# Kernel tuning notes

Hardware: AMD Instinct MI355X
Metric: run time of the kernel (lower is better)

## Reference

```python
import jax, jax.numpy as jnp
import numpy as np

N = 20000; DX = 512; DW = 64; DY = 256; M = 320000
DS = DX // 2; DD = DX // 4; DP = DS + DD  # 256, 128, 384
EPS = 1e-9; LN_EPS = 1e-5; SLOPE = 0.05
PNAMES = ['rW1','rb1','rg1','rbt1','rW2','rb2','yW1','yb1','yg1','ybt1','yW2','yb2',
          'iaW1','iab1','iag1','iabt1','iaW2','iab2','cW1','cb1','cg1','cbt1','cW2','cb2']

def _mlp2(h, W1, b1, g, be, W2, b2):
    # Linear -> LayerNorm -> LeakyReLU(0.05) -> Linear  (matches mlp(..., norm='layer'))
    h = h @ W1 + b1
    mu = jnp.mean(h, axis=-1, keepdims=True)
    var = jnp.mean((h - mu) ** 2, axis=-1, keepdims=True)
    h = (h - mu) * jax.lax.rsqrt(var + LN_EPS) * g + be
    h = jnp.where(h >= 0, h, SLOPE * h)
    return h @ W2 + b2

def _m(Pp, n, h):
    return _mlp2(h, Pp[n+'W1'], Pp[n+'b1'], Pp[n+'g1'], Pp[n+'bt1'], Pp[n+'W2'], Pp[n+'b2'])

def _agg(a, b):
    s = a + b
    return jnp.where(s >= 0, s, SLOPE * s)

def _run(x, ei, edge_attr, u_r, u_ia, u_pick, Pp, dec=None):
    """GuoUnpool forward (steps 1a, 2a, 2b). ei: concrete numpy [2,M] int64.
    dec holds concrete sampled decisions; built from the uniforms when None."""
    build = dec is None
    if build:
        dec = {}
    # coalesce (edges are duplicate-free) + lexsort by (src, dst)
    perm = np.argsort(ei[0].astype(np.int64) * N + ei[1].astype(np.int64), kind='stable')
    src, dst = ei[0][perm], ei[1][perm]
    ea = edge_attr[perm]
    # --- step 1a: bernoulli unpool decision per node (I_s = I_u = empty, I_r = all nodes)
    pr = jax.nn.sigmoid(_m(Pp, 'r', x)[:, 0])
    if build:
        dec['choose'] = np.asarray(u_r) < np.asarray(pr)
    choose = dec['choose']
    Iu = np.flatnonzero(choose); Is = np.flatnonzero(~choose)
    logP = jnp.sum(jnp.where(jnp.asarray(choose), jnp.log(pr + EPS), jnp.log(1.0 - pr + EPS)))
    prs = jnp.clip(pr, EPS, 1.0 - EPS)
    ent = -jnp.sum(prs * jnp.log(prs) + (1.0 - prs) * jnp.log(1.0 - prs))
    # --- projections (_ps1_idx = [0:ds+D], _ps2_idx = [0:ds] + [ds+D:ds+2D]) and child embeddings
    ps1 = x[:, :DP]
    ps2 = jnp.concatenate([x[:, :DS], x[:, DS + DD:DS + 2 * DD]], axis=-1)
    y1 = _m(Pp, 'y', ps1)   # [N, dy]; rows at Is give x_static, rows at Iu give x_c1
    y2 = _m(Pp, 'y', ps2)   # rows at Iu give x_c2
    x_out = jnp.concatenate([y1[Is], y1[Iu], y2[Iu]], axis=0)
    # --- step 2a: intra-edge decision for unpooled nodes
    p_ia = jax.nn.sigmoid(_m(Pp, 'ia', _agg(y1[Iu], y2[Iu]))[:, 0])
    if build:
        dec['vc'] = np.asarray(u_ia)[Iu] < np.asarray(p_ia)
    vc = dec['vc']
    logP = logP + jnp.sum(jnp.where(jnp.asarray(vc), jnp.log(p_ia + EPS), jnp.log(1.0 - p_ia + EPS)))
    ps = jnp.clip(p_ia, EPS, 1.0 - EPS)
    ent = ent - jnp.sum(ps * jnp.log(ps) + (1.0 - ps) * jnp.log(1.0 - ps))
    # --- step 2b: categorical neighbor pick for unpooled nodes without intra edge
    if build:
        iun = Iu[~vc]
        par = np.concatenate([src, dst]); nb = np.concatenate([dst, src])
        ek = np.concatenate([np.arange(len(src)), np.arange(len(src))])
        keep = np.zeros(N, dtype=bool); keep[iun] = True
        msk = keep[par]
        par, nb, ek = par[msk], nb[msk], ek[msk]
        o = np.lexsort((nb, par))  # adj lists sorted by neighbor id, grouped by parent
        par, nb, ek = par[o], nb[o], ek[o]
        new = np.r_[True, par[1:] != par[:-1]]
        dec['par'], dec['nb'], dec['ek'] = par, nb, ek
        dec['seg'] = np.cumsum(new) - 1
        dec['starts'] = np.flatnonzero(new)
    par, nb, ek = dec['par'], dec['nb'], dec['ek']
    segn, starts = dec['seg'], dec['starts']
    Pn = len(par); nseg = int(segn[-1]) + 1
    seg = jnp.asarray(segn)
    yagg = _agg(y1, y2)
    feats = jnp.concatenate([yagg[par], ea[ek], x[nb]], axis=-1)  # [Pn, dy+dw+dx]
    scores = _m(Pp, 'c', feats)[:, 0]
    mx = jax.ops.segment_max(scores, seg, num_segments=nseg)
    e = jnp.exp(scores - mx[segn])
    den = jax.ops.segment_sum(e, seg, num_segments=nseg)
    probs = e / den[segn]                      # per-parent softmax over neighbors
    if build:
        # multinomial pick via inverse CDF on the provided per-parent uniform
        p_np = np.asarray(probs).astype(np.float64)
        cum = np.cumsum(p_np)
        base = np.concatenate([[0.0], cum])[starts]
        cumw = cum - base[segn]
        useg = np.asarray(u_pick)[par[starts]][segn]
        cand = np.where(cumw > useg, np.arange(Pn), Pn)
        pick = np.minimum.reduceat(cand, starts)
        last = np.r_[starts[1:] - 1, Pn - 1]
        dec['pick'] = np.minimum(pick, last)
    pick = dec['pick']
    logP = logP + jnp.sum(jnp.log(jnp.clip(probs[pick], EPS, None)))
    pc = jnp.clip(probs, EPS, None)
    ent = ent - jnp.sum(pc * jnp.log(pc))
    return (x_out, logP, ent), dec

def _init_params(key):
    Pp = {}
    specs = [('r', DX, max(1, DX // 2), 1), ('y', DP, 128, DY), ('ia', DY, 128, 1), ('c', DY + DW + DX, 128, 1)]
    ks = jax.random.split(key, len(specs))
    for (n, a, h, o), k in zip(specs, ks):
        k1, k2 = jax.random.split(k)
        Pp[n+'W1'] = jax.random.normal(k1, (a, h), jnp.float32) / np.sqrt(a)
        Pp[n+'b1'] = jnp.zeros((h,), jnp.float32)
        Pp[n+'g1'] = jnp.ones((h,), jnp.float32)
        Pp[n+'bt1'] = jnp.zeros((h,), jnp.float32)
        Pp[n+'W2'] = jax.random.normal(k2, (h, o), jnp.float32) / np.sqrt(h)
        Pp[n+'b2'] = jnp.zeros((o,), jnp.float32)
    return Pp

def setup_inputs() -> dict:
    key = jax.random.key(0)
    k = jax.random.split(key, 6)
    x = jax.random.normal(k[0], (N, DX), jnp.float32)
    rng = np.random.default_rng(0)
    ns = int(M * 1.5)
    s = rng.integers(0, N, ns); d = rng.integers(0, N, ns)
    ok = s != d; s, d = s[ok], d[ok]
    _, ui = np.unique(s.astype(np.int64) * N + d, return_index=True)  # duplicate-free (coalesced)
    sel = rng.permutation(ui)[:M]
    edge_index = jnp.asarray(np.stack([s[sel], d[sel]]).astype(np.int64))
    inp = {
        'x': x,
        'edge_index': edge_index,
        'edge_attr': 0.5 * jax.random.normal(k[1], (M, DW), jnp.float32),
        'u_r': jax.random.uniform(k[2], (N,), jnp.float32),
        'u_ia': jax.random.uniform(k[3], (N,), jnp.float32),
        'u_pick': jax.random.uniform(k[4], (N,), jnp.float32),
    }
    inp.update(_init_params(k[5]))
    return inp

def reference(x, edge_index, edge_attr, u_r, u_ia, u_pick,
              rW1, rb1, rg1, rbt1, rW2, rb2,
              yW1, yb1, yg1, ybt1, yW2, yb2,
              iaW1, iab1, iag1, iabt1, iaW2, iab2,
              cW1, cb1, cg1, cbt1, cW2, cb2):
    Pp = dict(zip(PNAMES, (rW1, rb1, rg1, rbt1, rW2, rb2, yW1, yb1, yg1, ybt1, yW2, yb2,
                           iaW1, iab1, iag1, iabt1, iaW2, iab2, cW1, cb1, cg1, cbt1, cW2, cb2)))
    out, _ = _run(x, np.asarray(edge_index), edge_attr, u_r, u_ia, u_pick, Pp)
    return out
```

## Files before the change

kernel.cpp:

```cpp
#include <hip/hip_runtime.h>
#include <math.h>

#define KN 20000
#define KM 320000

typedef __attribute__((ext_vector_type(8))) short bf16x8;
typedef __attribute__((ext_vector_type(4))) float f32x4;

__device__ __forceinline__ ushort f2bf(float f){
  union{float f; unsigned u;} a; a.f=f;
  unsigned r = a.u + 0x7FFFu + ((a.u>>16)&1u);
  return (ushort)(r>>16);
}
__device__ __forceinline__ float bf2f(ushort u){
  union{unsigned u; float f;} a; a.u=((unsigned)u)<<16; return a.f;
}

__device__ __forceinline__ void blk_add2(double lp, double en, double* acc, double* sh){
#pragma unroll
  for (int o=32;o;o>>=1){ lp+=__shfl_xor(lp,o,64); en+=__shfl_xor(en,o,64); }
  int w=threadIdx.x>>6;
  if ((threadIdx.x&63)==0){ sh[2*w]=lp; sh[2*w+1]=en; }
  __syncthreads();
  if (threadIdx.x==0){
    double L=0,E=0; int nw=(blockDim.x+63)>>6;
    for (int i=0;i<nw;i++){L+=sh[2*i];E+=sh[2*i+1];}
    atomicAdd(&acc[0],L); atomicAdd(&acc[1],E);
  }
  __syncthreads();
}

__global__ __launch_bounds__(256) void k_prep_all(
    const float* __restrict__ x, ushort* __restrict__ x_hi, ushort* __restrict__ x_lo,
    const float* __restrict__ Wr1, ushort* __restrict__ Wrt_hi, ushort* __restrict__ Wrt_lo,
    double* __restrict__ w1d,
    const float* __restrict__ Wc1, ushort* __restrict__ W1t,
    const float* __restrict__ Wy1, ushort* __restrict__ W1yt,
    const float* __restrict__ Wy2, ushort* __restrict__ W2yt,
    int* __restrict__ deg,int* __restrict__ fill,int* __restrict__ keep,
    int* __restrict__ counters,double* __restrict__ acc){
  int i=blockIdx.x*256+threadIdx.x;
  if (i<KN*512/8){
    const float* s=x+(size_t)i*8;
    union{ushort u[8]; uint4 v;} oh, ol;
#pragma unroll
    for (int j=0;j<8;j++){
      float v=s[j];
      ushort h=f2bf(v);
      oh.u[j]=h;
      ol.u[j]=f2bf(v-bf2f(h));
    }
    *(uint4*)(x_hi+(size_t)i*8)=oh.v;
    *(uint4*)(x_lo+(size_t)i*8)=ol.v;
  }
  if (i<512*256){
    w1d[i]=(double)Wr1[i];
    int n=i&255, k=i>>8;
    float wv=Wr1[(size_t)k*256+n];
    ushort h=f2bf(wv);
    int kt=k>>5, kc=(k>>3)&3, j=k&7;
    size_t dst=(((size_t)kt*1024)+(size_t)kc*256+(size_t)n)*8+j;
    Wrt_hi[dst]=h;
    Wrt_lo[dst]=f2bf(wv-bf2f(h));
  }
  if (i<832*128){
    int n=i&127, k=i>>7;
    W1t[(size_t)n*832+k]=f2bf(Wc1[(size_t)k*128+n]);
  }
  if (i<384*128){
    int n=i&127, k=i>>7;
    W1yt[(size_t)n*384+k]=f2bf(Wy1[(size_t)k*128+n]);
  }
  if (i<128*256){
    int n=i&255, k=i>>8;
    W2yt[(size_t)n*128+k]=f2bf(Wy2[(size_t)k*256+n]);
  }
  if (i<KN){ deg[i]=0; fill[i]=0; keep[i]=0; }
  if (i<8) counters[i]=0;
  if (i<2) acc[i]=0.0;
}

#define RFLAG_TAU 3e-4f
#define YEXTP 261
__global__ __launch_bounds__(512) void k_mega1(const float* __restrict__ x,
    const ushort* __restrict__ x_hi,const ushort* __restrict__ x_lo,
    const ushort* __restrict__ Wrt_hi,const ushort* __restrict__ Wrt_lo,
    const double* __restrict__ w1d,
    const float* __restrict__ b1,const float* __restrict__ g1,
    const float* __restrict__ bt1,const float* __restrict__ W2,const float* __restrict__ b2,
    const float* __restrict__ u_r, float* __restrict__ pr, int* __restrict__ choose,
    const ushort* __restrict__ W1t, float* __restrict__ hxP,
    const ushort* __restrict__ W1yt,const float* __restrict__ b1y,const float* __restrict__ g1y,
    const float* __restrict__ bt1y,const ushort* __restrict__ W2yt,const float* __restrict__ b2y,
    float* __restrict__ y1_f,float* __restrict__ y2_f,
    float* __restrict__ yagg_f,ushort* __restrict__ yagg_bf,
    int RB,int HXB){
  __shared__ __align__(16) ushort Bl[2][2][8192];
  __shared__ float psum[64][2], pvar[64][2], pdot[64][2];
  __shared__ int flagsh[64];
  __shared__ double dsh[256];
  int t=threadIdx.x;
  int w=t>>6, l=t&63;
  int lr=l&15, lk=l>>4;
  if ((int)blockIdx.x>=RB+HXB){
    int b=blockIdx.x-RB-HXB;
    int sub=t>>8, tt=t&255;
    char* gbase=(char*)Bl + sub*25600;
    float*  hf  =(float*)gbase;
    float*  yext=(float*)gbase;
    ushort* hb  =(ushort*)(gbase+16896);
    int wy=tt>>6, ly=tt&63;
    int lry=ly&15, lky=ly>>4;
    int md=wy&1, kh=wy>>1;
    int row0=(b*2+sub)*16;
    const ushort* xr=x_hi+(size_t)(row0+lry)*512;
    f32x4 acc1[8];
#pragma unroll
    for (int c=0;c<8;c++) acc1[c]=(f32x4){0,0,0,0};
#pragma unroll
    for (int kt=0;kt<6;kt++){
      int k0=kh*192+kt*32+lky*8;
      int ks=(md && k0>=256)? k0+128 : k0;
      bf16x8 a=*(const bf16x8*)(xr+ks);
#pragma unroll
      for (int c=0;c<8;c++){
        bf16x8 b_=*(const bf16x8*)(W1yt+(size_t)(c*16+lry)*384+k0);
        acc1[c]=__builtin_amdgcn_mfma_f32_16x16x32_bf16(a,b_,acc1[c],0,0,0);
      }
    }
    if (kh==0){
#pragma unroll
      for (int i=0;i<4;i++){
        int row=lky*4+i;
#pragma unroll
        for (int c=0;c<8;c++) hf[((size_t)md*16+row)*132+c*16+lry]=acc1[c][i];
      }
    }
    __syncthreads();
    if (kh==1){
      float b1v[8],g1v[8],btv[8];
#pragma unroll
      for (int c=0;c<8;c++){ int col=c*16+lry; b1v[c]=b1y[col]; g1v[c]=g1y[col]; btv[c]=bt1y[col]; }
#pragma unroll
      for (int i=0;i<4;i++){
        int row=lky*4+i;
        float hv[8]; float s=0.f;
#pragma unroll
        for (int c=0;c<8;c++){ hv[c]=acc1[c][i]+hf[((size_t)md*16+row)*132+c*16+lry]+b1v[c]; s+=hv[c]; }
#pragma unroll
        for (int o=8;o;o>>=1) s+=__shfl_xor(s,o,64);
        float mu=s*(1.0f/128.0f);
        float v=0.f;
#pragma unroll
        for (int c=0;c<8;c++){ float d=hv[c]-mu; v+=d*d; }
#pragma unroll
        for (int o=8;o;o>>=1) v+=__shfl_xor(v,o,64);
        float rs=1.0f/sqrtf(v*(1.0f/128.0f)+1e-5f);
        ushort* hrow=hb+((size_t)md*16+row)*136;
#pragma unroll
        for (int c=0;c<8;c++){
          float hn=(hv[c]-mu)*rs*g1v[c]+btv[c];
          hn=hn>=0.f?hn:0.05f*hn;
          hrow[c*16+lry]=f2bf(hn);
        }
      }
    }
    __syncthreads();
    f32x4 acc2[8];
#pragma unroll
    for (int c=0;c<8;c++) acc2[c]=(f32x4){0,0,0,0};
    const ushort* ha=hb+((size_t)md*16+lry)*136;
#pragma unroll
    for (int kt=0;kt<4;kt++){
      bf16x8 a=*(const bf16x8*)(ha+kt*32+lky*8);
#pragma unroll
      for (int c=0;c<8;c++){
        bf16x8 b_=*(const bf16x8*)(W2yt+(size_t)(kh*128+c*16+lry)*128+kt*32+lky*8);
        acc2[c]=__builtin_amdgcn_mfma_f32_16x16x32_bf16(a,b_,acc2[c],0,0,0);
      }
    }
    float b2v[8];
#pragma unroll
    for (int c=0;c<8;c++) b2v[c]=b2y[kh*128+c*16+lry];
    if (md==0){
#pragma unroll
      for (int i=0;i<4;i++){
        int row=lky*4+i;
#pragma unroll
        for (int c=0;c<8;c++) yext[(size_t)row*YEXTP+kh*128+c*16+lry]=acc2[c][i]+b2v[c];
      }
    }
    __syncthreads();
    if (md==0){
#pragma unroll
      for (int i=0;i<4;i++){
        int row=lky*4+i, n=row0+row;
        float* orow=y1_f+(size_t)n*256+kh*128;
#pragma unroll
        for (int c=0;c<8;c++) orow[c*16+lry]=acc2[c][i]+b2v[c];
      }
    } else {
#pragma unroll
      for (int i=0;i<4;i++){
        int row=lky*4+i, n=row0+row;
        size_t base=(size_t)n*256+kh*128;
#pragma unroll
        for (int c=0;c<8;c++){
          int colk=c*16+lry;
          float v2=acc2[c][i]+b2v[c];
          float v1=yext[(size_t)row*YEXTP+kh*128+colk];
          float ga=v1+v2; ga=ga>=0.f?ga:0.05f*ga;
          yagg_f[base+colk]=ga;
          yagg_bf[base+colk]=f2bf(ga);
          y2_f[base+colk]=v2;
        }
      }
    }
    return;
  }
  if ((int)blockIdx.x>=RB){
    int b2=blockIdx.x-RB;
    int rh=w>>2, cw=w&3;
    int row0=b2*32+rh*16;
    const ushort* ar=x_hi+(size_t)(row0+lr)*512;
    f32x4 acc3[2];
#pragma unroll
    for (int c=0;c<2;c++) acc3[c]=(f32x4){0,0,0,0};
#pragma unroll
    for (int kt=0;kt<16;kt++){
      bf16x8 a=*(const bf16x8*)(ar+320+kt*32+lk*8);
#pragma unroll
      for (int c=0;c<2;c++){
        bf16x8 b=*(const bf16x8*)(W1t+(size_t)(cw*32+c*16+lr)*832+320+kt*32+lk*8);
        acc3[c]=__builtin_amdgcn_mfma_f32_16x16x32_bf16(a,b,acc3[c],0,0,0);
      }
    }
#pragma unroll
    for (int i=0;i<4;i++){
      int n=row0+lk*4+i;
      float2 v; v.x=acc3[0][i]; v.y=acc3[1][i];
      *(float2*)(hxP+(size_t)n*128+lr*8+cw*2)=v;
    }
    return;
  }
  int rg=w>>1, ch=w&1;
  int row0=blockIdx.x*64;
  if (t<64) flagsh[t]=0;
  int q0=t*2, q1=t*2+1;
  f32x4 acc[8];
#pragma unroll
  for (int c=0;c<8;c++) acc[c]=(f32x4){0,0,0,0};
  int rowA=row0+rg*16+lr; if (rowA>=KN) rowA=KN-1;
  const ushort* ah=x_hi+(size_t)rowA*512;
  const ushort* al=x_lo+(size_t)rowA*512;
  bf16x8 nh0=*(const bf16x8*)(Wrt_hi+q0*8);
  bf16x8 nh1=*(const bf16x8*)(Wrt_hi+q1*8);
  bf16x8 nl0=*(const bf16x8*)(Wrt_lo+q0*8);
  bf16x8 nl1=*(const bf16x8*)(Wrt_lo+q1*8);
  *(bf16x8*)&Bl[0][0][q0*8]=nh0; *(bf16x8*)&Bl[0][0][q1*8]=nh1;
  *(bf16x8*)&Bl[0][1][q0*8]=nl0; *(bf16x8*)&Bl[0][1][q1*8]=nl1;
  nh0=*(const bf16x8*)(Wrt_hi+8192+q0*8);
  nh1=*(const bf16x8*)(Wrt_hi+8192+q1*8);
  nl0=*(const bf16x8*)(Wrt_lo+8192+q0*8);
  nl1=*(const bf16x8*)(Wrt_lo+8192+q1*8);
  bf16x8 a_h0=*(const bf16x8*)(ah+0*32+lk*8), a_l0=*(const bf16x8*)(al+0*32+lk*8);
  bf16x8 a_h1=*(const bf16x8*)(ah+1*32+lk*8), a_l1=*(const bf16x8*)(al+1*32+lk*8);
  bf16x8 a_h2=*(const bf16x8*)(ah+2*32+lk*8), a_l2=*(const bf16x8*)(al+2*32+lk*8);
  bf16x8 a_h3=*(const bf16x8*)(ah+3*32+lk*8), a_l3=*(const bf16x8*)(al+3*32+lk*8);
  __syncthreads();
#define RBODY(KT,AH,AL) { \
    const int cur_=(KT)&1, nxt_=cur_^1; \
    if ((KT)<15){ \
      *(bf16x8*)&Bl[nxt_][0][q0*8]=nh0; *(bf16x8*)&Bl[nxt_][0][q1*8]=nh1; \
      *(bf16x8*)&Bl[nxt_][1][q0*8]=nl0; *(bf16x8*)&Bl[nxt_][1][q1*8]=nl1; \
      if ((KT)<14){ \
        size_t so_=(size_t)((KT)+2)*8192; \
        nh0=*(const bf16x8*)(Wrt_hi+so_+q0*8); nh1=*(const bf16x8*)(Wrt_hi+so_+q1*8); \
        nl0=*(const bf16x8*)(Wrt_lo+so_+q0*8); nl1=*(const bf16x8*)(Wrt_lo+so_+q1*8); \
      } \
    } \
    bf16x8 uh_=AH, ul_=AL; \
    if ((KT)<12){ \
      int ko_=((KT)+4)*32+lk*8; \
      AH=*(const bf16x8*)(ah+ko_); \
      AL=*(const bf16x8*)(al+ko_); \
    } \
    _Pragma("unroll") \
    for (int c=0;c<8;c++){ \
      int col_=ch*128+c*16+lr; \
      bf16x8 vh_=*(const bf16x8*)&Bl[cur_][0][((lk<<8)+col_)*8]; \
      bf16x8 vl_=*(const bf16x8*)&Bl[cur_][1][((lk<<8)+col_)*8]; \
      acc[c]=__builtin_amdgcn_mfma_f32_16x16x32_bf16(uh_,vh_,acc[c],0,0,0); \
      acc[c]=__builtin_amdgcn_mfma_f32_16x16x32_bf16(uh_,vl_,acc[c],0,0,0); \
      acc[c]=__builtin_amdgcn_mfma_f32_16x16x32_bf16(ul_,vh_,acc[c],0,0,0); \
    } \
    __syncthreads(); \
  }
  RBODY(0,a_h0,a_l0)  RBODY(1,a_h1,a_l1)  RBODY(2,a_h2,a_l2)  RBODY(3,a_h3,a_l3)
  RBODY(4,a_h0,a_l0)  RBODY(5,a_h1,a_l1)  RBODY(6,a_h2,a_l2)  RBODY(7,a_h3,a_l3)
  RBODY(8,a_h0,a_l0)  RBODY(9,a_h1,a_l1)  RBODY(10,a_h2,a_l2) RBODY(11,a_h3,a_l3)
  RBODY(12,a_h0,a_l0) RBODY(13,a_h1,a_l1) RBODY(14,a_h2,a_l2) RBODY(15,a_h3,a_l3)
#undef RBODY
  float b1v[8],g1v[8],btv[8],w2v[8];
#pragma unroll
  for (int c=0;c<8;c++){
    int col=ch*128+c*16+lr;
    b1v[c]=b1[col]; g1v[c]=g1[col]; btv[c]=bt1[col]; w2v[c]=W2[col];
  }
  float hv[4][8];
#pragma unroll
  for (int i=0;i<4;i++){
    float s=0.f;
#pragma unroll
    for (int c=0;c<8;c++){ hv[i][c]=acc[c][i]+b1v[c]; s+=hv[i][c]; }
#pragma unroll
    for (int o=8;o;o>>=1) s+=__shfl_xor(s,o,64);
    if (lr==0) psum[rg*16+lk*4+i][ch]=s;
  }
  __syncthreads();
  float mu_[4];
#pragma unroll
  for (int i=0;i<4;i++){
    int r=rg*16+lk*4+i;
    mu_[i]=(psum[r][0]+psum[r][1])*(1.0f/256.0f);
    float v=0.f;
#pragma unroll
    for (int c=0;c<8;c++){ float d=hv[i][c]-mu_[i]; v+=d*d; }
#pragma unroll
    for (int o=8;o;o>>=1) v+=__shfl_xor(v,o,64);
    if (lr==0) pvar[r][ch]=v;
  }
  __syncthreads();
#pragma unroll
  for (int i=0;i<4;i++){
    int r=rg*16+lk*4+i;
    float rs=1.0f/sqrtf((pvar[r][0]+pvar[r][1])*(1.0f/256.0f)+1e-5f);
    float dot=0.f;
#pragma unroll
    for (int c=0;c<8;c++){
      float hn=(hv[i][c]-mu_[i])*rs*g1v[c]+btv[c];
      hn=hn>=0.f?hn:0.05f*hn;
      dot=fmaf(hn,w2v[c],dot);
    }
#pragma unroll
    for (int o=8;o;o>>=1) dot+=__shfl_xor(dot,o,64);
    if (lr==0) pdot[r][ch]=dot;
  }
  __syncthreads();
  if (t<64){
    int n=row0+t;
    if (n<KN){
      float o2=pdot[t][0]+pdot[t][1]+b2[0];
      float pf=1.0f/(1.0f+expf(-o2));
      float u=u_r[n];
      pr[n]=pf;
      choose[n]=(u<pf)?1:0;
      if (fabsf(pf-u)<RFLAG_TAU) flagsh[t]=1;
    }
  }
  __syncthreads();
  for (int r=0;r<64;r++){
    if (!flagsh[r]) continue;
    int n=row0+r;
    if (t<256){
      double ha=(double)b1[t];
      const float* xr=x+(size_t)n*512;
      for (int k=0;k<512;k++) ha=fma((double)xr[k],w1d[(size_t)k*256+t],ha);
      dsh[t]=ha;
    }
    __syncthreads();
    if (t<64){
      double s=0;
      for (int j=t;j<256;j+=64) s+=dsh[j];
#pragma unroll
      for (int o=32;o;o>>=1) s+=__shfl_xor(s,o,64);
      double mu=s*(1.0/256.0);
      double v=0;
      for (int j=t;j<256;j+=64){ double d=dsh[j]-mu; v+=d*d; }
#pragma unroll
      for (int o=32;o;o>>=1) v+=__shfl_xor(v,o,64);
      double rs=1.0/sqrt(v*(1.0/256.0)+1e-5);
      double dot=0;
      for (int j=t;j<256;j+=64){
        double hn=(dsh[j]-mu)*rs*(double)g1[j]+(double)bt1[j];
        hn = hn>=0.0? hn : 0.05*hn;
        dot=fma(hn,(double)W2[j],dot);
      }
#pragma unroll
      for (int o=32;o;o>>=1) dot+=__shfl_xor(dot,o,64);
      if (t==0){
        double p=1.0/(1.0+exp(-(dot+(double)b2[0])));
        float pf=(float)p;
        pr[n]=pf;
        choose[n]=(u_r[n]<pf)?1:0;
      }
    }
    __syncthreads();
  }
}

__global__ __launch_bounds__(1024) void k_scan_choose(const int* __restrict__ choose,int* __restrict__ excl,
                                                      int* __restrict__ iu,int* __restrict__ counters){
  __shared__ int wsum[16], woff[16];
  const int CH=(KN+1023)/1024;
  int t=threadIdx.x, lane=t&63, wid=t>>6;
  int base=t*CH;
  int s=0;
  for (int i=0;i<CH;i++){int idx=base+i; if (idx<KN) s+=choose[idx];}
  int inc=s;
  for (int o=1;o<64;o<<=1){ int v=__shfl_up(inc,o,64); if (lane>=o) inc+=v; }
  if (lane==63) wsum[wid]=inc;
  __syncthreads();
  if (t==0){ int r=0; for (int i=0;i<16;i++){ woff[i]=r; r+=wsum[i]; } counters[2]=r; }
  __syncthreads();
  int ex=woff[wid]+inc-s;
  for (int i=0;i<CH;i++){
    int idx=base+i;
    if (idx<KN){ int c=choose[idx]; excl[idx]=ex; if (c) iu[ex]=idx; ex+=c; }
  }
}

__global__ __launch_bounds__(256) void k_mega2(const float* __restrict__ yagg_f,
    const ushort* __restrict__ yagg_bf,const ushort* __restrict__ W1t,float* __restrict__ hyP,
    const int* __restrict__ iu,const float* __restrict__ u_ia,
    const float* __restrict__ W1,const float* __restrict__ b1,const float* __restrict__ g1,
    const float* __restrict__ bt1,const float* __restrict__ W2,const float* __restrict__ b2,
    float* __restrict__ p_ia,int* __restrict__ vc,int* __restrict__ keep,double* __restrict__ acc,
    const float* __restrict__ y1_f,const float* __restrict__ y2_f,
    const int* __restrict__ choose,const int* __restrict__ excl,
    float* __restrict__ out,const float* __restrict__ pr,
    int cnt,int HB,int IAB,int SCB){
  __shared__ float insh[16][256];
  __shared__ float hsh[16][128];
  __shared__ double sh[8];
  int t=threadIdx.x;
  int w=t>>6, l=t&63;
  int lr=l&15, lk=l>>4;
  if ((int)blockIdx.x<HB){
    int rh=w>>1, cq=w&1;
    int row0=blockIdx.x*32+rh*16;
    const ushort* ar=yagg_bf+(size_t)(row0+lr)*256+lk*8;
    f32x4 acc4[4];
#pragma unroll
    for (int c=0;c<4;c++) acc4[c]=(f32x4){0,0,0,0};
#pragma unroll
    for (int kt=0;kt<8;kt++){
      bf16x8 a=*(const bf16x8*)(ar+kt*32);
#pragma unroll
      for (int c=0;c<4;c++){
        bf16x8 b=*(const bf16x8*)(W1t+(size_t)(cq*64+c*16+lr)*832+kt*32+lk*8);
        acc4[c]=__builtin_amdgcn_mfma_f32_16x16x32_bf16(a,b,acc4[c],0,0,0);
      }
    }
#pragma unroll
    for (int i=0;i<4;i++){
      int n=row0+lk*4+i;
      float4 v; v.x=acc4[0][i]; v.y=acc4[1][i]; v.z=acc4[2][i]; v.w=acc4[3][i];
      *(float4*)(hyP+(size_t)n*128+lr*8+cq*4)=v;
    }
    return;
  }
  if ((int)blockIdx.x<HB+IAB){
    int row0=(blockIdx.x-HB)*16;
    for (int i=t;i<16*256;i+=256){
      int r=i>>8,k=i&255;
      int row=row0+r;
      if (row<cnt){
        unsigned n=(unsigned)iu[row];
        if (n<KN) insh[r][k]=yagg_f[(size_t)n*256+k];
        else insh[r][k]=0.f;
      }
    }
    __syncthreads();
    int h=t>>7, tt=t&127;
    float accv[8]; float bb=b1[tt];
#pragma unroll
    for (int r=0;r<8;r++) accv[r]=bb;
    for (int k=0;k<256;k+=4){
      float w0=W1[(k+0)*128+tt],w1=W1[(k+1)*128+tt],w2=W1[(k+2)*128+tt],w3=W1[(k+3)*128+tt];
#pragma unroll
      for (int r=0;r<8;r++){
        float4 f=*(const float4*)&insh[h*8+r][k];
        accv[r]=fmaf(f.x,w0,accv[r]); accv[r]=fmaf(f.y,w1,accv[r]); accv[r]=fmaf(f.z,w2,accv[r]); accv[r]=fmaf(f.w,w3,accv[r]);
      }
    }
#pragma unroll
    for (int r=0;r<8;r++) hsh[h*8+r][tt]=accv[r];
    __syncthreads();
    int g=t>>4, tl=t&15;
    float hv[8];
#pragma unroll
    for (int j=0;j<8;j++) hv[j]=hsh[g][tl+16*j];
    float s=0;
#pragma unroll
    for (int j=0;j<8;j++) s+=hv[j];
#pragma unroll
    for (int o=8;o;o>>=1) s+=__shfl_xor(s,o,64);
    float mu=s*(1.0f/128.0f);
    float v=0;
#pragma unroll
    for (int j=0;j<8;j++){float d=hv[j]-mu; v+=d*d;}
#pragma unroll
    for (int o=8;o;o>>=1) v+=__shfl_xor(v,o,64);
    float rs=1.0f/sqrtf(v*(1.0f/128.0f)+1e-5f);
    float dot=0;
#pragma unroll
    for (int j=0;j<8;j++){
      int idx=tl+16*j;
      float hn=(hv[j]-mu)*rs*g1[idx]+bt1[idx];
      hn=hn>=0.f?hn:0.05f*hn;
      dot=fmaf(hn,W2[idx],dot);
    }
#pragma unroll
    for (int o=8;o;o>>=1) dot+=__shfl_xor(dot,o,64);
    double lp=0,en=0;
    if (tl==0){
      int row=row0+g;
      if (row<cnt){
        unsigned n=(unsigned)iu[row];
        if (n<KN){
          float o=dot+b2[0];
          double p=1.0/(1.0+exp(-(double)o));
          float pf=(float)p;
          p_ia[row]=pf;
          int vv=(u_ia[n]<pf)?1:0;
          vc[row]=vv;
          if(!vv) keep[n]=1;
          lp = vv? log((double)pf+1e-9) : log(1.0-(double)pf+1e-9);
          double ps=fmin(fmax((double)pf,1e-9),1.0-1e-9);
          en = -(ps*log(ps)+(1.0-ps)*log(1.0-ps));
        }
      }
    }
    blk_add2(lp,en,acc,sh);
    return;
  }
  if ((int)blockIdx.x<HB+IAB+SCB){
    int b=blockIdx.x-HB-IAB;
    int r0=b*32;
    for (int r=0;r<32;r++){
      int n=r0+r;
      if (n>=KN) break;
      int cch=choose[n], ex=excl[n];
      int r1 = cch? (KN-cnt)+ex : n-ex;
      if (r1>=0 && r1<KN+cnt) out[(size_t)r1*256+t]=y1_f[(size_t)n*256+t];
      if (cch){ int r2=KN+ex; if (r2<KN+cnt) out[(size_t)r2*256+t]=y2_f[(size_t)n*256+t]; }
    }
    return;
  }
  {
    int i=(blockIdx.x-HB-IAB-SCB)*256+t;
    double lp=0,en=0;
    if (i<KN){
      double p=(double)pr[i];
      lp = choose[i]? log(p+1e-9) : log(1.0-p+1e-9);
      double ps=fmin(fmax(p,1e-9),1.0-1e-9);
      en = -(ps*log(ps)+(1.0-ps)*log(1.0-ps));
    }
    blk_add2(lp,en,acc,(double*)insh);
  }
}

__global__ void k_count(const int* __restrict__ ei,const int* __restrict__ keep,int* __restrict__ deg){
  int e=blockIdx.x*256+threadIdx.x;
  if (e<KM){
    int s=ei[e], d=ei[KM+e];
    if (keep[s]) atomicAdd(&deg[s],1);
    if (keep[d]) atomicAdd(&deg[d],1);
  }
}

__global__ __launch_bounds__(1024) void k_scan_deg(const int* __restrict__ deg,int* __restrict__ boff,
                                                   int* __restrict__ nodeseg,int* __restrict__ counters){
  __shared__ int wsum[16], woff[16];
  const int CH=(KN+1023)/1024;
  int t=threadIdx.x, lane=t&63, wid=t>>6;
  int base=t*CH;
  int s=0, sc=0;
  for (int i=0;i<CH;i++){int idx=base+i; if(idx<KN){ int d=deg[idx]; s+=d; sc+=(d>0)?1:0; }}
  int inc=s;
  for (int o=1;o<64;o<<=1){ int v=__shfl_up(inc,o,64); if (lane>=o) inc+=v; }
  if (lane==63) wsum[wid]=inc;
  __syncthreads();
  if (t==0){ int r=0; for (int i=0;i<16;i++){ woff[i]=r; r+=wsum[i]; } boff[KN]=r; counters[0]=r; }
  __syncthreads();
  int ex=woff[wid]+inc-s;
  for (int i=0;i<CH;i++){int idx=base+i; if(idx<KN){ boff[idx]=ex; ex+=deg[idx]; }}
  __syncthreads();
  int inc2=sc;
  for (int o=1;o<64;o<<=1){ int v=__shfl_up(inc2,o,64); if (lane>=o) inc2+=v; }
  if (lane==63) wsum[wid]=inc2;
  __syncthreads();
  if (t==0){ int r=0; for (int i=0;i<16;i++){ woff[i]=r; r+=wsum[i]; } counters[1]=r; }
  __syncthreads();
  int ex2=woff[wid]+inc2-sc;
  for (int i=0;i<CH;i++){int idx=base+i; if(idx<KN && deg[idx]>0){ nodeseg[ex2]=idx; ex2++; }}
}

__global__ void k_fill(const int* __restrict__ ei,const int* __restrict__ keep,const int* __restrict__ boff,
                       int* __restrict__ fill,int* __restrict__ parA,int* __restrict__ keyA,int* __restrict__ ekA){
  int e=blockIdx.x*256+threadIdx.x;
  if (e<KM){
    int s=ei[e], d=ei[KM+e];
    if (keep[s]){ int pos=boff[s]+atomicAdd(&fill[s],1); parA[pos]=s; keyA[pos]=d*2;   ekA[pos]=e; }
    if (keep[d]){ int pos=boff[d]+atomicAdd(&fill[d],1); parA[pos]=d; keyA[pos]=s*2+1; ekA[pos]=e; }
  }
}

__global__ void k_rank(const int* __restrict__ parA,const int* __restrict__ keyA,const int* __restrict__ ekA,
                       const int* __restrict__ boff,const int* __restrict__ counters,
                       int* __restrict__ parS,int* __restrict__ nbS,int* __restrict__ ekS){
  int i=blockIdx.x*256+threadIdx.x;
  int Pn=counters[0];
  if (i<Pn){
    int par=parA[i], key=keyA[i];
    int lo=boff[par], hi=boff[par+1];
    int rank=0;
    for (int j=lo;j<hi;j++) rank += (keyA[j]<key)?1:0;
    int pos=lo+rank;
    parS[pos]=par; nbS[pos]=key>>1; ekS[pos]=ekA[i];
  }
}

__global__ __launch_bounds__(256) void k_cscore_v6(
    const float* __restrict__ ea,const float* __restrict__ hyP,const float* __restrict__ hxP,
    const int* __restrict__ parS,const int* __restrict__ nbS,const int* __restrict__ ekS,
    const int* __restrict__ counters,
    const ushort* __restrict__ W1t,const float* __restrict__ b1,const float* __restrict__ g1,
    const float* __restrict__ bt1,const float* __restrict__ W2,const float* __restrict__ b2,
    float* __restrict__ scores){
  int Pn=counters[0];
  if (Pn<=0) return;
  int t=threadIdx.x;
  int w=t>>6, l=t&63;
  int lr=l&15, lk=l>>4;
  float b2s=b2[0];
  float b1v[8],g1v[8],btv[8],w2v[8];
#pragma unroll
  for (int c=0;c<8;c++){
    int col=c*16+lr;
    b1v[c]=b1[col]; g1v[c]=g1[col]; btv[c]=bt1[col]; w2v[c]=W2[col];
  }
  int ngrp=(Pn+63)>>6;
  for (int g=blockIdx.x; g<ngrp; g+=gridDim.x){
    int p0=g*64+w*16;
    float hs[4][8];
#pragma unroll
    for (int i=0;i<4;i++){
      int p=p0+lk*4+i; int pc=p<Pn?p:Pn-1;
      const float* hyp=hyP+(size_t)parS[pc]*128+lr*8;
      const float* hxp=hxP+(size_t)nbS[pc]*128+lr*8;
      float4 ya=*(const float4*)hyp, yb=*(const float4*)(hyp+4);
      float4 xa=*(const float4*)hxp, xb=*(const float4*)(hxp+4);
      hs[i][0]=ya.x+xa.x; hs[i][1]=ya.y+xa.y; hs[i][2]=ya.z+xa.z; hs[i][3]=ya.w+xa.w;
      hs[i][4]=yb.x+xb.x; hs[i][5]=yb.y+xb.y; hs[i][6]=yb.z+xb.z; hs[i][7]=yb.w+xb.w;
    }
    int pA=p0+lr; int ca=pA<Pn?pA:Pn-1;
    const float* eaA=ea+(size_t)ekS[ca]*64;
    f32x4 acc[8];
#pragma unroll
    for (int c=0;c<8;c++) acc[c]=(f32x4){0,0,0,0};
#pragma unroll
    for (int kt=0;kt<2;kt++){
      float4 fa=*(const float4*)(eaA+kt*32+lk*8);
      float4 fb=*(const float4*)(eaA+kt*32+lk*8+4);
      union{ushort u[8]; bf16x8 v;} A;
      A.u[0]=f2bf(fa.x); A.u[1]=f2bf(fa.y); A.u[2]=f2bf(fa.z); A.u[3]=f2bf(fa.w);
      A.u[4]=f2bf(fb.x); A.u[5]=f2bf(fb.y); A.u[6]=f2bf(fb.z); A.u[7]=f2bf(fb.w);
      bf16x8 a=A.v;
#pragma unroll
      for (int c=0;c<8;c++){
        bf16x8 b=*(const bf16x8*)(W1t+(size_t)(c*16+lr)*832+256+kt*32+lk*8);
        acc[c]=__builtin_amdgcn_mfma_f32_16x16x32_bf16(a,b,acc[c],0,0,0);
      }
    }
#pragma unroll
    for (int i=0;i<4;i++){
      float hv[8]; float s=0.f;
#pragma unroll
      for (int c=0;c<8;c++){ hv[c]=acc[c][i]+hs[i][c]+b1v[c]; s+=hv[c]; }
#pragma unroll
      for (int o=8;o;o>>=1) s+=__shfl_xor(s,o,64);
      float mu=s*(1.0f/128.0f);
      float v=0.f;
#pragma unroll
      for (int c=0;c<8;c++){ float d=hv[c]-mu; v+=d*d; }
#pragma unroll
      for (int o=8;o;o>>=1) v+=__shfl_xor(v,o,64);
      float rs=1.0f/sqrtf(v*(1.0f/128.0f)+1e-5f);
      float dot=0.f;
#pragma unroll
      for (int c=0;c<8;c++){
        float hn=(hv[c]-mu)*rs*g1v[c]+btv[c];
        hn=hn>=0.f?hn:0.05f*hn;
        dot=fmaf(hn,w2v[c],dot);
      }
#pragma unroll
      for (int o=8;o;o>>=1) dot+=__shfl_xor(dot,o,64);
      if (lr==0){
        int prow=p0+lk*4+i;
        if (prow<Pn) scores[prow]=dot+b2s;
      }
    }
  }
}

__global__ __launch_bounds__(256) void k_segment(const float* __restrict__ scores,const int* __restrict__ boff,
    const int* __restrict__ nodeseg,int* __restrict__ counters,const float* __restrict__ u_pick,
    double* __restrict__ acc,float* __restrict__ out,int cnt){
  __shared__ double sh[8];
  int nseg=counters[1];
  int s=blockIdx.x*256+threadIdx.x;
  double lp=0,en=0;
  if (s<nseg){
    int n=nodeseg[s];
    int lo=boff[n],hi=boff[n+1];
    float mx=-1e30f;
    for (int p=lo;p<hi;p++) mx=fmaxf(mx,scores[p]);
    float den=0;
    for (int p=lo;p<hi;p++) den+=expf(scores[p]-mx);
    double u=(double)u_pick[n];
    double cum=0; float ppick=-1.f; float plast=0.f;
    for (int p=lo;p<hi;p++){
      float e=expf(scores[p]-mx);
      float prob=e/den;
      double pc=fmax((double)prob,1e-9);
      en -= pc*log(pc);
      plast=prob;
      if (ppick<0.f){ cum+=(double)prob; if (cum>u) ppick=prob; }
    }
    if (ppick<0.f) ppick=plast;
    lp=log(fmax((double)ppick,1e-9));
  }
  blk_add2(lp,en,acc,sh);
  if (threadIdx.x==0){
    __threadfence();
    int done=atomicAdd(&counters[3],1);
    if (done==(int)gridDim.x-1){
      __threadfence();
      size_t base=(size_t)(KN+cnt)*256;
      out[base]=(float)acc[0];
      out[base+1]=(float)acc[1];
    }
  }
}

extern "C" void kernel_launch(void* const* d_in,const int* in_sizes,int n_in,
                              void* d_out,int out_size,void* d_ws,size_t ws_size,
                              hipStream_t stream){
  const float* x     =(const float*)d_in[0];
  const int*   ei    =(const int*)  d_in[1];
  const float* ea    =(const float*)d_in[2];
  const float* u_r   =(const float*)d_in[3];
  const float* u_ia  =(const float*)d_in[4];
  const float* u_pick=(const float*)d_in[5];
  const float* Pp[24];
  for (int i=0;i<24;i++) Pp[i]=(const float*)d_in[6+i];
  float* out=(float*)d_out;
  int cnt=(out_size-2)/256 - KN;
  if (cnt<0) cnt=0;

  char* w=(char*)d_ws;
  size_t off=0;
  auto carve=[&](size_t bytes)->char*{ off=(off+255)&~(size_t)255; char* p=w+off; off+=bytes; return p; };
  int*    counters=(int*)   carve(64);
  double* acc     =(double*)carve(64);
  float*  pr      =(float*) carve((size_t)KN*4);
  int*    choose  =(int*)   carve((size_t)KN*4);
  int*    excl    =(int*)   carve((size_t)KN*4);
  int*    iu      =(int*)   carve((size_t)KN*4);
  float*  p_ia    =(float*) carve((size_t)KN*4);
  int*    vc      =(int*)   carve((size_t)KN*4);
  int*    keep    =(int*)   carve((size_t)KN*4);
  int*    deg     =(int*)   carve((size_t)KN*4);
  int*    fill    =(int*)   carve((size_t)KN*4);
  int*    boff    =(int*)   carve((size_t)(KN+1)*4);
  int*    nodeseg =(int*)   carve((size_t)KN*4);
  int*    parA    =(int*)   carve((size_t)2*KM*4);
  int*    keyA    =(int*)   carve((size_t)2*KM*4);
  int*    ekA     =(int*)   carve((size_t)2*KM*4);
  int*    parS    =(int*)   carve((size_t)2*KM*4);
  int*    nbS     =(int*)   carve((size_t)2*KM*4);
  int*    ekS     =(int*)   carve((size_t)2*KM*4);
  float*  scores  =(float*) carve((size_t)2*KM*4);
  float*  yagg_f  =(float*) carve((size_t)KN*256*4);
  ushort* yagg_bf =(ushort*)carve((size_t)KN*256*2);
  float*  y1_f    =(float*) carve((size_t)KN*256*4);
  float*  y2_f    =(float*) carve((size_t)KN*256*4);
  ushort* x_bf    =(ushort*)carve((size_t)KN*512*2);
  ushort* x_lo    =(ushort*)carve((size_t)KN*512*2);
  ushort* W1t     =(ushort*)carve((size_t)832*128*2);
  double* w1d     =(double*)carve((size_t)512*256*8);
  ushort* W1yt    =(ushort*)carve((size_t)128*384*2);
  ushort* W2yt    =(ushort*)carve((size_t)256*128*2);
  ushort* Wrt_hi  =(ushort*)carve((size_t)256*512*2);
  ushort* Wrt_lo  =(ushort*)carve((size_t)256*512*2);
  float*  hy      =(float*) carve((size_t)KN*128*4);
  float*  hx      =(float*) carve((size_t)KN*128*4);
  (void)ws_size;(void)n_in;(void)in_sizes;

  const int RB=(KN+63)/64;
  const int HXB=KN/32;
  const int YB2=KN/32;
  const int HB=KN/32;
  const int IAB=(cnt+15)/16;
  const int SCB=(KN+31)/32;
  const int NTB=(KN+255)/256;

  k_prep_all<<<(KN*512/8+255)/256,256,0,stream>>>(x,x_bf,x_lo,
      Pp[0],Wrt_hi,Wrt_lo,w1d, Pp[18],W1t, Pp[6],W1yt, Pp[10],W2yt,
      deg,fill,keep,counters,acc);
  k_mega1<<<RB+HXB+YB2,512,0,stream>>>(x,x_bf,x_lo,Wrt_hi,Wrt_lo,w1d,
      Pp[1],Pp[2],Pp[3],Pp[4],Pp[5],u_r,pr,choose,W1t,hx,
      W1yt,Pp[7],Pp[8],Pp[9],W2yt,Pp[11],y1_f,y2_f,yagg_f,yagg_bf,RB,HXB);
  k_scan_choose<<<1,1024,0,stream>>>(choose,excl,iu,counters);
  k_mega2<<<HB+IAB+SCB+NTB,256,0,stream>>>(yagg_f,yagg_bf,W1t,hy,iu,u_ia,
      Pp[12],Pp[13],Pp[14],Pp[15],Pp[16],Pp[17],p_ia,vc,keep,acc,
      y1_f,y2_f,choose,excl,out,pr,cnt,HB,IAB,SCB);
  k_count<<<(KM+255)/256,256,0,stream>>>(ei,keep,deg);
  k_scan_deg<<<1,1024,0,stream>>>(deg,boff,nodeseg,counters);
  k_fill<<<(KM+255)/256,256,0,stream>>>(ei,keep,boff,fill,parA,keyA,ekA);
  k_rank<<<(2*KM+255)/256,256,0,stream>>>(parA,keyA,ekA,boff,counters,parS,nbS,ekS);
  k_cscore_v6<<<2560,256,0,stream>>>(ea,hy,hx,parS,nbS,ekS,counters,W1t,Pp[19],Pp[20],Pp[21],Pp[22],Pp[23],scores);
  k_segment<<<(KN+255)/256,256,0,stream>>>(scores,boff,nodeseg,counters,u_pick,acc,out,cnt);
}
```

Before: 407.8 us.

## Fuse edge-sort, scoring and segment-softmax tail into one cooperative kernel

Replaces the six tail kernels (degree count, degree scan, fill, rank, edge scoring and segment softmax) with a single cooperative kernel. The stages are separated by grid-wide syncs and use grid-stride loops, with the grid sized from occupancy and cached in a static. This removes several launch gaps and kernel-boundary drains. In exchange it adds grid.sync costs, moves the degree scan onto one 256-thread block instead of 1024 threads, and may give the scoring stage fewer resident blocks than before.

```diff
diff --git a/kernel.cpp b/kernel.cpp
--- a/kernel.cpp
+++ b/kernel.cpp
@@ -1,8 +1,11 @@
 #include <hip/hip_runtime.h>
+#include <hip/hip_cooperative_groups.h>
 #include <math.h>
 
 #define KN 20000
 #define KM 320000
+
+namespace cg = cooperative_groups;
 
 typedef __attribute__((ext_vector_type(8))) short bf16x8;
 typedef __attribute__((ext_vector_type(4))) float f32x4;
@@ -561,187 +564,180 @@
   }
 }
 
-__global__ void k_count(const int* __restrict__ ei,const int* __restrict__ keep,int* __restrict__ deg){
-  int e=blockIdx.x*256+threadIdx.x;
-  if (e<KM){
+__global__ __launch_bounds__(256) void k_tail(
+    const int* __restrict__ ei,const int* __restrict__ keep,int* __restrict__ deg,
+    int* __restrict__ boff,int* __restrict__ nodeseg,int* __restrict__ counters,
+    int* __restrict__ fill,int* __restrict__ parA,int* __restrict__ keyA,int* __restrict__ ekA,
+    int* __restrict__ parS,int* __restrict__ nbS,int* __restrict__ ekS,
+    const float* __restrict__ ea,const float* __restrict__ hyP,const float* __restrict__ hxP,
+    const ushort* __restrict__ W1t,const float* __restrict__ b1,const float* __restrict__ g1,
+    const float* __restrict__ bt1,const float* __restrict__ W2,const float* __restrict__ b2,
+    float* __restrict__ scores,const float* __restrict__ u_pick,
+    double* __restrict__ acc,float* __restrict__ out,int cnt){
+  cg::grid_group grid = cg::this_grid();
+  __shared__ int wsum[4], woff[4];
+  __shared__ double sh[8];
+  int t=threadIdx.x;
+  int gsz=gridDim.x;
+  for (int e=blockIdx.x*256+t; e<KM; e+=gsz*256){
     int s=ei[e], d=ei[KM+e];
     if (keep[s]) atomicAdd(&deg[s],1);
     if (keep[d]) atomicAdd(&deg[d],1);
   }
-}
-
-__global__ __launch_bounds__(1024) void k_scan_deg(const int* __restrict__ deg,int* __restrict__ boff,
-                                                   int* __restrict__ nodeseg,int* __restrict__ counters){
-  __shared__ int wsum[16], woff[16];
-  const int CH=(KN+1023)/1024;
-  int t=threadIdx.x, lane=t&63, wid=t>>6;
-  int base=t*CH;
-  int s=0, sc=0;
-  for (int i=0;i<CH;i++){int idx=base+i; if(idx<KN){ int d=deg[idx]; s+=d; sc+=(d>0)?1:0; }}
-  int inc=s;
-  for (int o=1;o<64;o<<=1){ int v=__shfl_up(inc,o,64); if (lane>=o) inc+=v; }
-  if (lane==63) wsum[wid]=inc;
-  __syncthreads();
-  if (t==0){ int r=0; for (int i=0;i<16;i++){ woff[i]=r; r+=wsum[i]; } boff[KN]=r; counters[0]=r; }
-  __syncthreads();
-  int ex=woff[wid]+inc-s;
-  for (int i=0;i<CH;i++){int idx=base+i; if(idx<KN){ boff[idx]=ex; ex+=deg[idx]; }}
-  __syncthreads();
-  int inc2=sc;
-  for (int o=1;o<64;o<<=1){ int v=__shfl_up(inc2,o,64); if (lane>=o) inc2+=v; }
-  if (lane==63) wsum[wid]=inc2;
-  __syncthreads();
-  if (t==0){ int r=0; for (int i=0;i<16;i++){ woff[i]=r; r+=wsum[i]; } counters[1]=r; }
-  __syncthreads();
-  int ex2=woff[wid]+inc2-sc;
-  for (int i=0;i<CH;i++){int idx=base+i; if(idx<KN && deg[idx]>0){ nodeseg[ex2]=idx; ex2++; }}
-}
-
-__global__ void k_fill(const int* __restrict__ ei,const int* __restrict__ keep,const int* __restrict__ boff,
-                       int* __restrict__ fill,int* __restrict__ parA,int* __restrict__ keyA,int* __restrict__ ekA){
-  int e=blockIdx.x*256+threadIdx.x;
-  if (e<KM){
+  grid.sync();
+  if (blockIdx.x==0){
+    const int CH=(KN+255)/256;
+    int lane=t&63, wid=t>>6;
+    int base=t*CH;
+    int s=0, sc=0;
+    for (int i=0;i<CH;i++){int idx=base+i; if(idx<KN){ int d=deg[idx]; s+=d; sc+=(d>0)?1:0; }}
+    int inc=s;
+    for (int o=1;o<64;o<<=1){ int v=__shfl_up(inc,o,64); if (lane>=o) inc+=v; }
+    if (lane==63) wsum[wid]=inc;
+    __syncthreads();
+    if (t==0){ int r=0; for (int i=0;i<4;i++){ woff[i]=r; r+=wsum[i]; } boff[KN]=r; counters[0]=r; }
+    __syncthreads();
+    int ex=woff[wid]+inc-s;
+    for (int i=0;i<CH;i++){int idx=base+i; if(idx<KN){ boff[idx]=ex; ex+=deg[idx]; }}
+    __syncthreads();
+    int inc2=sc;
+    for (int o=1;o<64;o<<=1){ int v=__shfl_up(inc2,o,64); if (lane>=o) inc2+=v; }
+    if (lane==63) wsum[wid]=inc2;
+    __syncthreads();
+    if (t==0){ int r=0; for (int i=0;i<4;i++){ woff[i]=r; r+=wsum[i]; } counters[1]=r; }
+    __syncthreads();
+    int ex2=woff[wid]+inc2-sc;
+    for (int i=0;i<CH;i++){int idx=base+i; if(idx<KN && deg[idx]>0){ nodeseg[ex2]=idx; ex2++; }}
+  }
+  grid.sync();
+  for (int e=blockIdx.x*256+t; e<KM; e+=gsz*256){
     int s=ei[e], d=ei[KM+e];
     if (keep[s]){ int pos=boff[s]+atomicAdd(&fill[s],1); parA[pos]=s; keyA[pos]=d*2;   ekA[pos]=e; }
     if (keep[d]){ int pos=boff[d]+atomicAdd(&fill[d],1); parA[pos]=d; keyA[pos]=s*2+1; ekA[pos]=e; }
   }
-}
-
-__global__ void k_rank(const int* __restrict__ parA,const int* __restrict__ keyA,const int* __restrict__ ekA,
-                       const int* __restrict__ boff,const int* __restrict__ counters,
-                       int* __restrict__ parS,int* __restrict__ nbS,int* __restrict__ ekS){
-  int i=blockIdx.x*256+threadIdx.x;
-  int Pn=counters[0];
-  if (i<Pn){
-    int par=parA[i], key=keyA[i];
-    int lo=boff[par], hi=boff[par+1];
-    int rank=0;
-    for (int j=lo;j<hi;j++) rank += (keyA[j]<key)?1:0;
-    int pos=lo+rank;
-    parS[pos]=par; nbS[pos]=key>>1; ekS[pos]=ekA[i];
-  }
-}
-
-__global__ __launch_bounds__(256) void k_cscore_v6(
-    const float* __restrict__ ea,const float* __restrict__ hyP,const float* __restrict__ hxP,
-    const int* __restrict__ parS,const int* __restrict__ nbS,const int* __restrict__ ekS,
-    const int* __restrict__ counters,
-    const ushort* __restrict__ W1t,const float* __restrict__ b1,const float* __restrict__ g1,
-    const float* __restrict__ bt1,const float* __restrict__ W2,const float* __restrict__ b2,
-    float* __restrict__ scores){
-  int Pn=counters[0];
-  if (Pn<=0) return;
-  int t=threadIdx.x;
-  int w=t>>6, l=t&63;
-  int lr=l&15, lk=l>>4;
-  float b2s=b2[0];
-  float b1v[8],g1v[8],btv[8],w2v[8];
-#pragma unroll
-  for (int c=0;c<8;c++){
-    int col=c*16+lr;
-    b1v[c]=b1[col]; g1v[c]=g1[col]; btv[c]=bt1[col]; w2v[c]=W2[col];
-  }
-  int ngrp=(Pn+63)>>6;
-  for (int g=blockIdx.x; g<ngrp; g+=gridDim.x){
-    int p0=g*64+w*16;
-    float hs[4][8];
-#pragma unroll
-    for (int i=0;i<4;i++){
-      int p=p0+lk*4+i; int pc=p<Pn?p:Pn-1;
-      const float* hyp=hyP+(size_t)parS[pc]*128+lr*8;
-      const float* hxp=hxP+(size_t)nbS[pc]*128+lr*8;
-      float4 ya=*(const float4*)hyp, yb=*(const float4*)(hyp+4);
-      float4 xa=*(const float4*)hxp, xb=*(const float4*)(hxp+4);
-      hs[i][0]=ya.x+xa.x; hs[i][1]=ya.y+xa.y; hs[i][2]=ya.z+xa.z; hs[i][3]=ya.w+xa.w;
-      hs[i][4]=yb.x+xb.x; hs[i][5]=yb.y+xb.y; hs[i][6]=yb.z+xb.z; hs[i][7]=yb.w+xb.w;
-    }
-    int pA=p0+lr; int ca=pA<Pn?pA:Pn-1;
-    const float* eaA=ea+(size_t)ekS[ca]*64;
-    f32x4 acc[8];
-#pragma unroll
-    for (int c=0;c<8;c++) acc[c]=(f32x4){0,0,0,0};
-#pragma unroll
-    for (int kt=0;kt<2;kt++){
-      float4 fa=*(const float4*)(eaA+kt*32+lk*8);
-      float4 fb=*(const float4*)(eaA+kt*32+lk*8+4);
-      union{ushort u[8]; bf16x8 v;} A;
-      A.u[0]=f2bf(fa.x); A.u[1]=f2bf(fa.y); A.u[2]=f2bf(fa.z); A.u[3]=f2bf(fa.w);
-      A.u[4]=f2bf(fb.x); A.u[5]=f2bf(fb.y); A.u[6]=f2bf(fb.z); A.u[7]=f2bf(fb.w);
-      bf16x8 a=A.v;
+  grid.sync();
+  {
+    int Pn=counters[0];
+    for (int i=blockIdx.x*256+t; i<Pn; i+=gsz*256){
+      int par=parA[i], key=keyA[i];
+      int lo=boff[par], hi=boff[par+1];
+      int rank=0;
+      for (int j=lo;j<hi;j++) rank += (keyA[j]<key)?1:0;
+      int pos=lo+rank;
+      parS[pos]=par; nbS[pos]=key>>1; ekS[pos]=ekA[i];
+    }
+  }
+  grid.sync();
+  {
+    int Pn=counters[0];
+    if (Pn>0){
+      int w=t>>6, l=t&63;
+      int lr=l&15, lk=l>>4;
+      float b2s=b2[0];
+      float b1v[8],g1v[8],btv[8],w2v[8];
 #pragma unroll
       for (int c=0;c<8;c++){
-        bf16x8 b=*(const bf16x8*)(W1t+(size_t)(c*16+lr)*832+256+kt*32+lk*8);
-        acc[c]=__builtin_amdgcn_mfma_f32_16x16x32_bf16(a,b,acc[c],0,0,0);
-      }
-    }
-#pragma unroll
-    for (int i=0;i<4;i++){
-      float hv[8]; float s=0.f;
-#pragma unroll
-      for (int c=0;c<8;c++){ hv[c]=acc[c][i]+hs[i][c]+b1v[c]; s+=hv[c]; }
-#pragma unroll
-      for (int o=8;o;o>>=1) s+=__shfl_xor(s,o,64);
-      float mu=s*(1.0f/128.0f);
-      float v=0.f;
-#pragma unroll
-      for (int c=0;c<8;c++){ float d=hv[c]-mu; v+=d*d; }
-#pragma unroll
-      for (int o=8;o;o>>=1) v+=__shfl_xor(v,o,64);
-      float rs=1.0f/sqrtf(v*(1.0f/128.0f)+1e-5f);
-      float dot=0.f;
-#pragma unroll
-      for (int c=0;c<8;c++){
-        float hn=(hv[c]-mu)*rs*g1v[c]+btv[c];
-        hn=hn>=0.f?hn:0.05f*hn;
-        dot=fmaf(hn,w2v[c],dot);
-      }
-#pragma unroll
-      for (int o=8;o;o>>=1) dot+=__shfl_xor(dot,o,64);
-      if (lr==0){
-        int prow=p0+lk*4+i;
-        if (prow<Pn) scores[prow]=dot+b2s;
-      }
-    }
-  }
-}
-
-__global__ __launch_bounds__(256) void k_segment(const float* __restrict__ scores,const int* __restrict__ boff,
-    const int* __restrict__ nodeseg,int* __restrict__ counters,const float* __restrict__ u_pick,
-    double* __restrict__ acc,float* __restrict__ out,int cnt){
-  __shared__ double sh[8];
-  int nseg=counters[1];
-  int s=blockIdx.x*256+threadIdx.x;
-  double lp=0,en=0;
-  if (s<nseg){
-    int n=nodeseg[s];
-    int lo=boff[n],hi=boff[n+1];
-    float mx=-1e30f;
-    for (int p=lo;p<hi;p++) mx=fmaxf(mx,scores[p]);
-    float den=0;
-    for (int p=lo;p<hi;p++) den+=expf(scores[p]-mx);
-    double u=(double)u_pick[n];
-    double cum=0; float ppick=-1.f; float plast=0.f;
-    for (int p=lo;p<hi;p++){
-      float e=expf(scores[p]-mx);
-      float prob=e/den;
-      double pc=fmax((double)prob,1e-9);
-      en -= pc*log(pc);
-      plast=prob;
-      if (ppick<0.f){ cum+=(double)prob; if (cum>u) ppick=prob; }
-    }
-    if (ppick<0.f) ppick=plast;
-    lp=log(fmax((double)ppick,1e-9));
-  }
-  blk_add2(lp,en,acc,sh);
-  if (threadIdx.x==0){
-    __threadfence();
-    int done=atomicAdd(&counters[3],1);
-    if (done==(int)gridDim.x-1){
-      __threadfence();
-      size_t base=(size_t)(KN+cnt)*256;
-      out[base]=(float)acc[0];
-      out[base+1]=(float)acc[1];
-    }
+        int col=c*16+lr;
+        b1v[c]=b1[col]; g1v[c]=g1[col]; btv[c]=bt1[col]; w2v[c]=W2[col];
+      }
+      int ngrp=(Pn+63)>>6;
+      for (int g=blockIdx.x; g<ngrp; g+=gsz){
+        int p0=g*64+w*16;
+        float hs[4][8];
+#pragma unroll
+        for (int i=0;i<4;i++){
+          int p=p0+lk*4+i; int pc=p<Pn?p:Pn-1;
+          const float* hyp=hyP+(size_t)parS[pc]*128+lr*8;
+          const float* hxp=hxP+(size_t)nbS[pc]*128+lr*8;
+          float4 ya=*(const float4*)hyp, yb=*(const float4*)(hyp+4);
+          float4 xa=*(const float4*)hxp, xb=*(const float4*)(hxp+4);
+          hs[i][0]=ya.x+xa.x; hs[i][1]=ya.y+xa.y; hs[i][2]=ya.z+xa.z; hs[i][3]=ya.w+xa.w;
+          hs[i][4]=yb.x+xb.x; hs[i][5]=yb.y+xb.y; hs[i][6]=yb.z+xb.z; hs[i][7]=yb.w+xb.w;
+        }
+        int pA=p0+lr; int ca=pA<Pn?pA:Pn-1;
+        const float* eaA=ea+(size_t)ekS[ca]*64;
+        f32x4 acc_[8];
+#pragma unroll
+        for (int c=0;c<8;c++) acc_[c]=(f32x4){0,0,0,0};
+#pragma unroll
+        for (int kt=0;kt<2;kt++){
+          float4 fa=*(const float4*)(eaA+kt*32+lk*8);
+          float4 fb=*(const float4*)(eaA+kt*32+lk*8+4);
+          union{ushort u[8]; bf16x8 v;} A;
+          A.u[0]=f2bf(fa.x); A.u[1]=f2bf(fa.y); A.u[2]=f2bf(fa.z); A.u[3]=f2bf(fa.w);
+          A.u[4]=f2bf(fb.x); A.u[5]=f2bf(fb.y); A.u[6]=f2bf(fb.z); A.u[7]=f2bf(fb.w);
+          bf16x8 a=A.v;
+#pragma unroll
+          for (int c=0;c<8;c++){
+            bf16x8 b=*(const bf16x8*)(W1t+(size_t)(c*16+lr)*832+256+kt*32+lk*8);
+            acc_[c]=__builtin_amdgcn_mfma_f32_16x16x32_bf16(a,b,acc_[c],0,0,0);
+          }
+        }
+#pragma unroll
+        for (int i=0;i<4;i++){
+          float hv[8]; float s=0.f;
+#pragma unroll
+          for (int c=0;c<8;c++){ hv[c]=acc_[c][i]+hs[i][c]+b1v[c]; s+=hv[c]; }
+#pragma unroll
+          for (int o=8;o;o>>=1) s+=__shfl_xor(s,o,64);
+          float mu=s*(1.0f/128.0f);
+          float v=0.f;
+#pragma unroll
+          for (int c=0;c<8;c++){ float d=hv[c]-mu; v+=d*d; }
+#pragma unroll
+          for (int o=8;o;o>>=1) v+=__shfl_xor(v,o,64);
+          float rs=1.0f/sqrtf(v*(1.0f/128.0f)+1e-5f);
+          float dot=0.f;
+#pragma unroll
+          for (int c=0;c<8;c++){
+            float hn=(hv[c]-mu)*rs*g1v[c]+btv[c];
+            hn=hn>=0.f?hn:0.05f*hn;
+            dot=fmaf(hn,w2v[c],dot);
+          }
+#pragma unroll
+          for (int o=8;o;o>>=1) dot+=__shfl_xor(dot,o,64);
+          if (lr==0){
+            int prow=p0+lk*4+i;
+            if (prow<Pn) scores[prow]=dot+b2s;
+          }
+        }
+      }
+    }
+  }
+  grid.sync();
+  {
+    int nseg=counters[1];
+    double lpT=0,enT=0;
+    for (int s0=blockIdx.x*256; s0<nseg; s0+=gsz*256){
+      int s=s0+t;
+      if (s<nseg){
+        int n=nodeseg[s];
+        int lo=boff[n],hi=boff[n+1];
+        float mx=-1e30f;
+        for (int p=lo;p<hi;p++) mx=fmaxf(mx,scores[p]);
+        float den=0;
+        for (int p=lo;p<hi;p++) den+=expf(scores[p]-mx);
+        double u=(double)u_pick[n];
+        double cum=0; float ppick=-1.f; float plast=0.f;
+        for (int p=lo;p<hi;p++){
+          float e=expf(scores[p]-mx);
+          float prob=e/den;
+          double pc=fmax((double)prob,1e-9);
+          enT -= pc*log(pc);
+          plast=prob;
+          if (ppick<0.f){ cum+=(double)prob; if (cum>u) ppick=prob; }
+        }
+        if (ppick<0.f) ppick=plast;
+        lpT+=log(fmax((double)ppick,1e-9));
+      }
+    }
+    blk_add2(lpT,enT,acc,sh);
+  }
+  grid.sync();
+  if (blockIdx.x==0 && t==0){
+    size_t base=(size_t)(KN+cnt)*256;
+    out[base]=(float)acc[0];
+    out[base+1]=(float)acc[1];
   }
 }
 
@@ -807,6 +803,20 @@
   const int SCB=(KN+31)/32;
   const int NTB=(KN+255)/256;
 
+  static int tail_blocks = 0;
+  if (tail_blocks==0){
+    int maxb=0;
+    if (hipOccupancyMaxActiveBlocksPerMultiprocessor(&maxb,(const void*)k_tail,256,0)!=hipSuccess || maxb<=0)
+      maxb=2;
+    hipDeviceProp_t prop; int dev=0;
+    hipGetDevice(&dev);
+    int ncu=256;
+    if (hipGetDeviceProperties(&prop,dev)==hipSuccess) ncu=prop.multiProcessorCount;
+    tail_blocks = maxb*ncu;
+    if (tail_blocks>2048) tail_blocks=2048;
+    if (tail_blocks<=0)   tail_blocks=512;
+  }
+
   k_prep_all<<<(KN*512/8+255)/256,256,0,stream>>>(x,x_bf,x_lo,
       Pp[0],Wrt_hi,Wrt_lo,w1d, Pp[18],W1t, Pp[6],W1yt, Pp[10],W2yt,
       deg,fill,keep,counters,acc);
@@ -817,10 +827,16 @@
   k_mega2<<<HB+IAB+SCB+NTB,256,0,stream>>>(yagg_f,yagg_bf,W1t,hy,iu,u_ia,
       Pp[12],Pp[13],Pp[14],Pp[15],Pp[16],Pp[17],p_ia,vc,keep,acc,
       y1_f,y2_f,choose,excl,out,pr,cnt,HB,IAB,SCB);
-  k_count<<<(KM+255)/256,256,0,stream>>>(ei,keep,deg);
-  k_scan_deg<<<1,1024,0,stream>>>(deg,boff,nodeseg,counters);
-  k_fill<<<(KM+255)/256,256,0,stream>>>(ei,keep,boff,fill,parA,keyA,ekA);
-  k_rank<<<(2*KM+255)/256,256,0,stream>>>(parA,keyA,ekA,boff,counters,parS,nbS,ekS);
-  k_cscore_v6<<<2560,256,0,stream>>>(ea,hy,hx,parS,nbS,ekS,counters,W1t,Pp[19],Pp[20],Pp[21],Pp[22],Pp[23],scores);
-  k_segment<<<(KN+255)/256,256,0,stream>>>(scores,boff,nodeseg,counters,u_pick,acc,out,cnt);
+  {
+    const float* W1c=Pp[19]; const float* b1c=Pp[20]; const float* g1c=Pp[21];
+    void* args[]={
+      (void*)&ei,(void*)&keep,(void*)&deg,(void*)&boff,(void*)&nodeseg,(void*)&counters,
+      (void*)&fill,(void*)&parA,(void*)&keyA,(void*)&ekA,
+      (void*)&parS,(void*)&nbS,(void*)&ekS,
+      (void*)&ea,(void*)&hy,(void*)&hx,
+      (void*)&W1t,(void*)&Pp[19],(void*)&Pp[20],(void*)&Pp[21],(void*)&Pp[22],(void*)&Pp[23],
+      (void*)&scores,(void*)&u_pick,(void*)&acc,(void*)&out,(void*)&cnt};
+    hipLaunchCooperativeKernel((void*)k_tail,dim3(tail_blocks),dim3(256),args,0,stream);
+    (void)W1c;(void)b1c;(void)g1c;
+  }
 }
```

New measurement: 619.6 us. +51.9%, slower.
